# Performance work log

Hardware: AMD Instinct MI355X
Metric: run time of the kernel (lower is better)

Reference implementation:

```python
import jax, jax.numpy as jnp
import numpy as np

B, S, D, H = 2, 2048, 1024, 16
HD = D // H  # head_dim = 64


def setup_inputs() -> dict:
    rng = jax.random.key(0)
    ks = jax.random.split(rng, 14)
    s = 0.02
    return {
        "query": jax.random.normal(ks[0], (B, S, D), jnp.float32),
        "key": jax.random.normal(ks[1], (B, S, D), jnp.float32),
        "value": jax.random.normal(ks[2], (B, S, D), jnp.float32),
        "Wq": jax.random.normal(ks[3], (D, D), jnp.float32) * s,
        "bq": jnp.zeros((D,), jnp.float32),
        "Wk": jax.random.normal(ks[4], (D, D), jnp.float32) * s,
        "bk": jnp.zeros((D,), jnp.float32),
        "Wv": jax.random.normal(ks[5], (D, D), jnp.float32) * s,
        "bv": jnp.zeros((D,), jnp.float32),
        "Wo": jax.random.normal(ks[6], (D, D), jnp.float32) * s,
        "bo": jnp.zeros((D,), jnp.float32),
        "Wa": jax.random.normal(ks[7], (3, D, D), jnp.float32) * s,  # 3 aspect projections
        "ba": jnp.zeros((3, D), jnp.float32),
    }


def reference(query, key, value, Wq, bq, Wk, bk, Wv, bv, Wo, bo, Wa, ba):
    scale = 1.0 / jnp.sqrt(jnp.asarray(HD, query.dtype))
    # projections; split heads -> [B, H, S, HD]
    q = (query @ Wq + bq).reshape(B, S, H, HD).transpose(0, 2, 1, 3)
    k = (key @ Wk + bk).reshape(B, S, H, HD).transpose(0, 2, 1, 3)
    v = (value @ Wv + bv).reshape(B, S, H, HD).transpose(0, 2, 1, 3)
    # main attention (dropout p=0, no masks)
    logits = jnp.einsum('bhqd,bhkd->bhqk', q, k) * scale
    attn_weights = jax.nn.softmax(logits, axis=-1)  # [B, H, S, S]
    ctx = jnp.einsum('bhqk,bhkd->bhqd', attn_weights, v)
    attn_output = ctx.transpose(0, 2, 1, 3).reshape(B, S, D) @ Wo + bo
    # 3 interpretable aspect patterns: each proj applied to query and key,
    # full-dim QK^T scaled by sqrt(head_dim), softmax over keys.
    q_asp = jnp.einsum('bsd,ade->abse', query, Wa) + ba[:, None, None, :]
    k_asp = jnp.einsum('bsd,ade->abse', key, Wa) + ba[:, None, None, :]
    pat_logits = jnp.einsum('abqd,abkd->abqk', q_asp, k_asp) * scale
    patterns = jax.nn.softmax(pat_logits, axis=-1)  # [3, B, S, S]
    return attn_output, attn_weights, patterns
```

## Files before the change

### kernel.cpp

```cpp
#include <hip/hip_runtime.h>

typedef unsigned short u16;
typedef short s16x4 __attribute__((ext_vector_type(4)));
typedef short s16x8 __attribute__((ext_vector_type(8)));
typedef float f32x4 __attribute__((ext_vector_type(4)));

#define DEVFN __device__ __forceinline__

constexpr long AW_OFF  = 4194304;
constexpr long PAT_OFF = AW_OFF + 134217728;

DEVFN u16 f2bf(float x) {
  unsigned u = __builtin_bit_cast(unsigned, x);
  unsigned r = (u + 0x7fffu + ((u >> 16) & 1u)) >> 16;
  return (u16)r;
}

DEVFN void gld16(const u16* g, u16* l) {
  __builtin_amdgcn_global_load_lds(
      (const __attribute__((address_space(1))) unsigned int*)g,
      (__attribute__((address_space(3))) unsigned int*)l, 16, 0, 0);
}

__global__ __launch_bounds__(256) void k_cvt3(const float* __restrict__ a,
                                              const float* __restrict__ b,
                                              const float* __restrict__ c,
                                              u16* __restrict__ out, int n4) {
  int i = blockIdx.x * 256 + threadIdx.x;
  if (i >= n4) return;
  const float* in = (blockIdx.y == 0) ? a : (blockIdx.y == 1) ? b : c;
  float4 v = ((const float4*)in)[i];
  s16x4 o; o[0] = f2bf(v.x); o[1] = f2bf(v.y); o[2] = f2bf(v.z); o[3] = f2bf(v.w);
  ((s16x4*)(out + (long)blockIdx.y * 4194304))[i] = o;
}

__global__ __launch_bounds__(256) void k_pack3(const float* __restrict__ a,
                                               const float* __restrict__ b,
                                               const float* __restrict__ c,
                                               float* __restrict__ out) {
  int i = blockIdx.x * 256 + threadIdx.x;
  const float* in = (i < 1024) ? a : (i < 2048) ? b : c;
  out[i] = in[i & 1023];
}

__global__ __launch_bounds__(256) void k_trW(const float* __restrict__ Wq,
                                             const float* __restrict__ Wk,
                                             const float* __restrict__ Wv,
                                             const float* __restrict__ Wo,
                                             const float* __restrict__ Wa,
                                             u16* __restrict__ Wqt,
                                             u16* __restrict__ Wot,
                                             u16* __restrict__ Wat) {
  __shared__ u16 tile[32][33];
  const int z = blockIdx.z;
  const float* in;
  u16* outp;
  if (z == 0)      { in = Wq; outp = Wqt; }
  else if (z == 1) { in = Wk; outp = Wqt + 1048576; }
  else if (z == 2) { in = Wv; outp = Wqt + 2097152; }
  else if (z == 3) { in = Wo; outp = Wot; }
  else             { in = Wa + (long)(z - 4) * 1048576; outp = Wat + (long)(z - 4) * 1048576; }
  int k0 = blockIdx.y * 32, n0 = blockIdx.x * 32;
  int tx = threadIdx.x & 31, ty = threadIdx.x >> 5;
#pragma unroll
  for (int i = 0; i < 4; ++i)
    tile[ty + i * 8][tx] = f2bf(in[(long)(k0 + ty + i * 8) * 1024 + (n0 + tx)]);
  __syncthreads();
#pragma unroll
  for (int i = 0; i < 4; ++i)
    outp[(long)(n0 + ty + i * 8) * 1024 + (k0 + tx)] = tile[tx][ty + i * 8];
}

template <bool IN_F32>
__global__ __launch_bounds__(256) void k_tr(const void* __restrict__ inv,
                                            u16* __restrict__ out,
                                            long ldin, long ldout,
                                            long inz1, long inz2, long outz, int zdiv) {
  __shared__ u16 tile[32][33];
  int z = blockIdx.z;
  long ioff = (long)(z / zdiv) * inz1 + (long)(z % zdiv) * inz2;
  int k0 = blockIdx.y * 32, n0 = blockIdx.x * 32;
  int tx = threadIdx.x, ty = threadIdx.y;
#pragma unroll
  for (int i = 0; i < 4; ++i) {
    long k = k0 + ty + i * 8, n = n0 + tx;
    u16 v;
    if constexpr (IN_F32) v = f2bf(((const float*)inv)[ioff + k * ldin + n]);
    else                  v = ((const u16*)inv)[ioff + k * ldin + n];
    tile[ty + i * 8][tx] = v;
  }
  __syncthreads();
  long ooff = (long)z * outz;
#pragma unroll
  for (int i = 0; i < 4; ++i) {
    long n = n0 + ty + i * 8, k = k0 + tx;
    out[ooff + n * ldout + k] = tile[tx][ty + i * 8];
  }
}

template <typename OutT, int EPI>
__global__ __launch_bounds__(256) void k_gemm_nt(
    const u16* __restrict__ Ap, const u16* __restrict__ Bp, OutT* __restrict__ Cp,
    const float* __restrict__ bias, const float* __restrict__ rinv, float alpha, int K,
    long lda, long ldb, long ldc,
    long saz1, long saz2, long sbz1, long sbz2, long scz1, long scz2,
    long sbias, int zdiv) {
  __shared__ __align__(16) u16 At[128][64];
  __shared__ __align__(16) u16 Bt[128][64];
  const int tid = threadIdx.x, lane = tid & 63, wid = tid >> 6;
  const int wm = wid >> 1, wn = wid & 1;

  const int gx = gridDim.x, gy = gridDim.y;
  int id = (blockIdx.z * gy + blockIdx.y) * gx + blockIdx.x;
  const int nb = gx * gy * (int)gridDim.z;
  if ((nb & 7) == 0) id = (id & 7) * (nb >> 3) + (id >> 3);
  const int bxi = id % gx, byi = (id / gx) % gy, bzi = id / (gx * gy);

  const int z = bzi, z1 = z / zdiv, z2 = z % zdiv;
  const u16* Ab = Ap + (long)z1 * saz1 + (long)z2 * saz2;
  const u16* Bb = Bp + (long)z1 * sbz1 + (long)z2 * sbz2;
  OutT* C = Cp + (long)z1 * scz1 + (long)z2 * scz2;
  const float* bv = bias ? bias + (long)z2 * sbias : nullptr;
  const int row0 = byi * 128, col0 = bxi * 128;
  const int lk = lane & 15, g = lane >> 4;

  f32x4 acc[4][4] = {};

  for (int k0 = 0; k0 < K; k0 += 64) {
#pragma unroll
    for (int it = 0; it < 4; ++it) {
      const int u = it * 256 + tid;
      const int r = u >> 3, p = u & 7;
      const int cg = (p ^ (r & 7)) * 8;
      gld16(Ab + (long)(row0 + r) * lda + (k0 + cg), &At[r][p * 8]);
      gld16(Bb + (long)(col0 + r) * ldb + (k0 + cg), &Bt[r][p * 8]);
    }
    __syncthreads();
#pragma unroll
    for (int kk = 0; kk < 2; ++kk) {
      s16x8 af[4], bf[4];
#pragma unroll
      for (int m = 0; m < 4; ++m)
        af[m] = *(const s16x8*)&At[wm * 64 + m * 16 + lk][((kk * 4 + g) ^ (lk & 7)) * 8];
#pragma unroll
      for (int n = 0; n < 4; ++n)
        bf[n] = *(const s16x8*)&Bt[wn * 64 + n * 16 + lk][((kk * 4 + g) ^ (lk & 7)) * 8];
#pragma unroll
      for (int m = 0; m < 4; ++m)
#pragma unroll
        for (int n = 0; n < 4; ++n)
          acc[m][n] = __builtin_amdgcn_mfma_f32_16x16x32_bf16(af[m], bf[n], acc[m][n], 0, 0, 0);
    }
    __syncthreads();
  }

  const float* rz = (EPI == 1) ? rinv + (long)z * 2048 : nullptr;
#pragma unroll
  for (int m = 0; m < 4; ++m) {
    const int grow = row0 + wm * 64 + m * 16 + g * 4;
#pragma unroll
    for (int r = 0; r < 4; ++r) {
      float iv = 0.0f;
      if constexpr (EPI == 1) iv = rz[grow + r];
#pragma unroll
      for (int n = 0; n < 4; ++n) {
        const int gcol = col0 + wn * 64 + n * 16 + lk;
        float v;
        if constexpr (EPI == 1) v = __expf(alpha * acc[m][n][r]) * iv;
        else                    v = alpha * acc[m][n][r] + (bv ? bv[gcol] : 0.0f);
        if constexpr (sizeof(OutT) == 2) C[(long)(grow + r) * ldc + gcol] = f2bf(v);
        else                             C[(long)(grow + r) * ldc + gcol] = v;
      }
    }
  }
}

template <typename OutT, int EPI>
__global__ __launch_bounds__(512, 1) void k_gemm8(
    const u16* __restrict__ Ap, const u16* __restrict__ Bp, OutT* __restrict__ Cp,
    const float* __restrict__ bias, const float* __restrict__ rinv, float alpha, int K,
    long lda, long ldb, long ldc,
    long saz1, long saz2, long sbz1, long sbz2, long scz1, long scz2,
    long sbias, int zdiv) {
  extern __shared__ __align__(16) u16 dyn[];
  u16* At = dyn;
  u16* Bt = dyn + 32768;
  const int tid = threadIdx.x, lane = tid & 63, wid = tid >> 6;
  const int wm = wid >> 2, wn = wid & 3;

  const int gx = gridDim.x, gy = gridDim.y;
  int id = (blockIdx.z * gy + blockIdx.y) * gx + blockIdx.x;
  const int nb = gx * gy * (int)gridDim.z;
  if ((nb & 7) == 0) id = (id & 7) * (nb >> 3) + (id >> 3);
  const int bxi = id % gx, byi = (id / gx) % gy, bzi = id / (gx * gy);

  const int z = bzi, z1 = z / zdiv, z2 = z % zdiv;
  const u16* Ab = Ap + (long)z1 * saz1 + (long)z2 * saz2;
  const u16* Bb = Bp + (long)z1 * sbz1 + (long)z2 * sbz2;
  OutT* C = Cp + (long)z1 * scz1 + (long)z2 * scz2;
  const float* bv = bias ? bias + (long)z2 * sbias : nullptr;
  const int row0 = byi * 256, col0 = bxi * 256;
  const int lk = lane & 15, g = lane >> 4;

  f32x4 acc[8][4] = {};
  const int NT = K >> 6;

  auto STAGE = [&](int t, int b) {
    const int k0 = t << 6;
#pragma unroll
    for (int it = 0; it < 4; ++it) {
      const int u = it * 512 + tid;
      const int r = u >> 3, p = u & 7;
      const int cg = (p ^ (r & 7)) * 8;
      gld16(Ab + (long)(row0 + r) * lda + (k0 + cg), At + b * 16384 + r * 64 + p * 8);
      gld16(Bb + (long)(col0 + r) * ldb + (k0 + cg), Bt + b * 16384 + r * 64 + p * 8);
    }
  };

  STAGE(0, 0);
  STAGE(1, 1);
  for (int t = 0; t < NT; ++t) {
    if (t + 1 < NT) asm volatile("s_waitcnt vmcnt(8)" ::: "memory");
    else            asm volatile("s_waitcnt vmcnt(0)" ::: "memory");
    __builtin_amdgcn_sched_barrier(0);
    __builtin_amdgcn_s_barrier();
    __builtin_amdgcn_sched_barrier(0);
    const u16* Ax = At + (t & 1) * 16384;
    const u16* Bx = Bt + (t & 1) * 16384;
#pragma unroll
    for (int kk = 0; kk < 2; ++kk) {
      s16x8 af[8], bf[4];
#pragma unroll
      for (int m = 0; m < 8; ++m)
        af[m] = *(const s16x8*)(Ax + (wm * 128 + m * 16 + lk) * 64 + ((kk * 4 + g) ^ (lk & 7)) * 8);
#pragma unroll
      for (int n = 0; n < 4; ++n)
        bf[n] = *(const s16x8*)(Bx + (wn * 64 + n * 16 + lk) * 64 + ((kk * 4 + g) ^ (lk & 7)) * 8);
#pragma unroll
      for (int m = 0; m < 8; ++m)
#pragma unroll
        for (int n = 0; n < 4; ++n)
          acc[m][n] = __builtin_amdgcn_mfma_f32_16x16x32_bf16(af[m], bf[n], acc[m][n], 0, 0, 0);
    }
    __builtin_amdgcn_sched_barrier(0);
    __builtin_amdgcn_s_barrier();
    __builtin_amdgcn_sched_barrier(0);
    if (t + 2 < NT) STAGE(t + 2, t & 1);
  }

  const float* rz = (EPI == 1) ? rinv + (long)z * 2048 : nullptr;
#pragma unroll
  for (int m = 0; m < 8; ++m) {
    const int grow = row0 + wm * 128 + m * 16 + g * 4;
#pragma unroll
    for (int r = 0; r < 4; ++r) {
      float iv = 0.0f;
      if constexpr (EPI == 1) iv = rz[grow + r];
#pragma unroll
      for (int n = 0; n < 4; ++n) {
        const int gcol = col0 + wn * 64 + n * 16 + lk;
        float v;
        if constexpr (EPI == 1) v = __expf(alpha * acc[m][n][r]) * iv;
        else                    v = alpha * acc[m][n][r] + (bv ? bv[gcol] : 0.0f);
        if constexpr (sizeof(OutT) == 2) C[(long)(grow + r) * ldc + gcol] = f2bf(v);
        else                             C[(long)(grow + r) * ldc + gcol] = v;
      }
    }
  }
}

__global__ __launch_bounds__(256) void k_flash(
    const u16* __restrict__ qp, const u16* __restrict__ kp, const u16* __restrict__ vt,
    u16* __restrict__ ctx, float* __restrict__ rinv) {
  __shared__ __align__(16) char lds[49152];
  u16* Qt = (u16*)lds;
  u16* Kt = (u16*)(lds + 16384);
  u16* Vl = (u16*)(lds + 32768);
  const int tid = threadIdx.x, lane = tid & 63, wid = tid >> 6;
  const int wk = wid >> 1, wq = wid & 1;

  const int gx = gridDim.x;
  int id = blockIdx.y * gx + blockIdx.x;
  const int nb = gx * (int)gridDim.y;
  if ((nb & 7) == 0) id = (id & 7) * (nb >> 3) + (id >> 3);
  const int bh = id / gx, q0 = (id % gx) * 128;

  const long qkbase = (long)(bh >> 4) * 2097152 + (long)(bh & 15) * 64;
  const long vbase = (long)bh * 131072;
  const int lk = lane & 15, g = lane >> 4;
  const int sp = lane & 7;
  const int sr = lane >> 3;

#pragma unroll
  for (int i = 0; i < 4; ++i) {
    const int rr = (wid * 4 + i) * 8 + sr;
    gld16(qp + qkbase + (long)(q0 + rr) * 1024 + ((sp ^ (rr & 7)) * 8), Qt + rr * 64 + sp * 8);
  }
  __syncthreads();

  s16x8 qf[2][4];
#pragma unroll
  for (int kk = 0; kk < 2; ++kk) {
#pragma unroll
    for (int nq = 0; nq < 4; ++nq)
      qf[kk][nq] = *(const s16x8*)(Qt + (wq * 64 + nq * 16 + lk) * 64 + ((kk * 4 + g) ^ (lk & 7)) * 8);
  }

  f32x4 cacc[4][4] = {};
  float rs[4] = {0.f, 0.f, 0.f, 0.f};

  for (int t = 0; t < 16; ++t) {
    const int kb = t * 128;
#pragma unroll
    for (int i = 0; i < 4; ++i) {
      const int rr = (wid * 4 + i) * 8 + sr;
      gld16(kp + qkbase + (long)(kb + rr) * 1024 + ((sp ^ (rr & 7)) * 8), Kt + rr * 64 + sp * 8);
      const int dd = (wid * 4 + i) * 4 + g;
      const int pv = lane & 15;
      const int cv = (pv & 8) | ((pv ^ dd) & 7);
      gld16(vt + vbase + (long)dd * 2048 + (kb + cv * 8), Vl + dd * 128 + pv * 8);
    }
    __syncthreads();

    f32x4 st[4][4] = {};
#pragma unroll
    for (int kk = 0; kk < 2; ++kk) {
      s16x8 af[4];
#pragma unroll
      for (int mk = 0; mk < 4; ++mk)
        af[mk] = *(const s16x8*)(Kt + (wk * 64 + mk * 16 + lk) * 64 + ((kk * 4 + g) ^ (lk & 7)) * 8);
#pragma unroll
      for (int mk = 0; mk < 4; ++mk)
#pragma unroll
        for (int nq = 0; nq < 4; ++nq)
          st[mk][nq] = __builtin_amdgcn_mfma_f32_16x16x32_bf16(af[mk], qf[kk][nq], st[mk][nq], 0, 0, 0);
    }
#pragma unroll
    for (int mk = 0; mk < 4; ++mk)
#pragma unroll
      for (int nq = 0; nq < 4; ++nq)
#pragma unroll
        for (int j = 0; j < 4; ++j) {
          const float p = __expf(st[mk][nq][j] * 0.125f);
          st[mk][nq][j] = p;
          rs[nq] += p;
        }
#pragma unroll
    for (int ks = 0; ks < 2; ++ks) {
      s16x8 pb[4];
#pragma unroll
      for (int nq = 0; nq < 4; ++nq) {
        s16x8 b;
#pragma unroll
        for (int j = 0; j < 4; ++j) {
          b[j]     = (short)f2bf(st[2 * ks][nq][j]);
          b[4 + j] = (short)f2bf(st[2 * ks + 1][nq][j]);
        }
        pb[nq] = b;
      }
#pragma unroll
      for (int md = 0; md < 4; ++md) {
        const int rowv = md * 16 + lk;
        const int u0 = ks * 4 + (g >> 1);
        const int p0 = wk * 8 + ((u0 ^ (rowv & 7)) & 7);
        const int p2 = wk * 8 + (((u0 + 2) ^ (rowv & 7)) & 7);
        const u16* vb0 = Vl + rowv * 128 + p0 * 8 + (g & 1) * 4;
        const u16* vb2 = Vl + rowv * 128 + p2 * 8 + (g & 1) * 4;
        s16x4 lo = *(const s16x4*)vb0;
        s16x4 hi = *(const s16x4*)vb2;
        s16x8 vf;
        vf[0] = lo[0]; vf[1] = lo[1]; vf[2] = lo[2]; vf[3] = lo[3];
        vf[4] = hi[0]; vf[5] = hi[1]; vf[6] = hi[2]; vf[7] = hi[3];
#pragma unroll
        for (int nq = 0; nq < 4; ++nq)
          cacc[md][nq] = __builtin_amdgcn_mfma_f32_16x16x32_bf16(vf, pb[nq], cacc[md][nq], 0, 0, 0);
      }
    }
    __syncthreads();
  }

#pragma unroll
  for (int nq = 0; nq < 4; ++nq) {
    rs[nq] += __shfl_xor(rs[nq], 16, 64);
    rs[nq] += __shfl_xor(rs[nq], 32, 64);
  }
  float* ctxl = (float*)lds;
  float* rsl  = (float*)(lds + 33024);
  if (wk == 1) {
#pragma unroll
    for (int md = 0; md < 4; ++md)
#pragma unroll
      for (int nq = 0; nq < 4; ++nq)
#pragma unroll
        for (int r = 0; r < 4; ++r)
          ctxl[(md * 16 + g * 4 + r) * 129 + wq * 64 + nq * 16 + lk] = cacc[md][nq][r];
    if (lane < 16)
#pragma unroll
      for (int nq = 0; nq < 4; ++nq) rsl[wq * 64 + nq * 16 + lane] = rs[nq];
  }
  __syncthreads();
  if (wk == 0) {
#pragma unroll
    for (int md = 0; md < 4; ++md)
#pragma unroll
      for (int nq = 0; nq < 4; ++nq)
#pragma unroll
        for (int r = 0; r < 4; ++r) {
          const int idx = (md * 16 + g * 4 + r) * 129 + wq * 64 + nq * 16 + lk;
          ctxl[idx] += cacc[md][nq][r];
        }
    if (lane < 16)
#pragma unroll
      for (int nq = 0; nq < 4; ++nq) {
        const int qi = wq * 64 + nq * 16 + lane;
        const float inv = 1.0f / (rsl[qi] + rs[nq]);
        rsl[qi] = inv;
        rinv[(long)bh * 2048 + q0 + qi] = inv;
      }
  }
  __syncthreads();
  const int qr = tid >> 1, half = tid & 1;
  const float inv = rsl[qr];
  u16* dst = ctx + (long)(bh >> 4) * 2097152 + (long)(q0 + qr) * 1024 + (long)(bh & 15) * 64 + half * 32;
#pragma unroll
  for (int c = 0; c < 4; ++c) {
    s16x8 o;
#pragma unroll
    for (int j = 0; j < 8; ++j) {
      const int d = half * 32 + c * 8 + j;
      o[j] = (short)f2bf(ctxl[d * 129 + qr] * inv);
    }
    ((s16x8*)dst)[c] = o;
  }
}

__global__ __launch_bounds__(256) void k_softmax(float* __restrict__ base) {
  float* p = base + (long)blockIdx.x * 2048;
  const int t = threadIdx.x;
  float4 v0 = ((const float4*)p)[t];
  float4 v1 = ((const float4*)p)[t + 256];
  float m = fmaxf(fmaxf(fmaxf(v0.x, v0.y), fmaxf(v0.z, v0.w)),
                  fmaxf(fmaxf(v1.x, v1.y), fmaxf(v1.z, v1.w)));
#pragma unroll
  for (int i = 32; i >= 1; i >>= 1) m = fmaxf(m, __shfl_xor(m, i, 64));
  __shared__ float sm[4], ss[4];
  if ((t & 63) == 0) sm[t >> 6] = m;
  __syncthreads();
  m = fmaxf(fmaxf(sm[0], sm[1]), fmaxf(sm[2], sm[3]));
  float4 e0, e1;
  e0.x = __expf(v0.x - m); e0.y = __expf(v0.y - m); e0.z = __expf(v0.z - m); e0.w = __expf(v0.w - m);
  e1.x = __expf(v1.x - m); e1.y = __expf(v1.y - m); e1.z = __expf(v1.z - m); e1.w = __expf(v1.w - m);
  float s = (e0.x + e0.y + e0.z + e0.w) + (e1.x + e1.y + e1.z + e1.w);
#pragma unroll
  for (int i = 32; i >= 1; i >>= 1) s += __shfl_xor(s, i, 64);
  if ((t & 63) == 0) ss[t >> 6] = s;
  __syncthreads();
  s = ss[0] + ss[1] + ss[2] + ss[3];
  float inv = 1.0f / s;
  e0.x *= inv; e0.y *= inv; e0.z *= inv; e0.w *= inv;
  e1.x *= inv; e1.y *= inv; e1.z *= inv; e1.w *= inv;
  ((float4*)p)[t] = e0;
  ((float4*)p)[t + 256] = e1;
}

extern "C" void kernel_launch(void* const* d_in, const int* in_sizes, int n_in,
                              void* d_out, int out_size, void* d_ws, size_t ws_size,
                              hipStream_t stream) {
  const float* query = (const float*)d_in[0];
  const float* key   = (const float*)d_in[1];
  const float* value = (const float*)d_in[2];
  const float* Wq = (const float*)d_in[3];
  const float* bq = (const float*)d_in[4];
  const float* Wk = (const float*)d_in[5];
  const float* bk = (const float*)d_in[6];
  const float* Wv = (const float*)d_in[7];
  const float* bv = (const float*)d_in[8];
  const float* Wo = (const float*)d_in[9];
  const float* bo = (const float*)d_in[10];
  const float* Wa = (const float*)d_in[11];
  const float* ba = (const float*)d_in[12];
  float* out = (float*)d_out;
  char* ws = (char*)d_ws;

  u16* qb  = (u16*)(ws + 0);
  u16* Wqt = (u16*)(ws + 25165824);
  u16* Wot = (u16*)(ws + 31457280);
  u16* Wat = (u16*)(ws + 33554432);
  u16* qp  = (u16*)(ws + 39845888);
  u16* kp  = (u16*)(ws + 48234496);
  u16* vp  = (u16*)(ws + 56623104);
  u16* vt  = (u16*)(ws + 65011712);
  u16* ctx = (u16*)(ws + 73400320);
  u16* qa  = (u16*)(ws + 81788928);
  float* rinv  = (float*)(ws + 25165824);
  float* pbias = (float*)(ws + 132120576);

  hipFuncSetAttribute((const void*)k_gemm8<u16, 0>,
                      hipFuncAttributeMaxDynamicSharedMemorySize, 131072);
  hipFuncSetAttribute((const void*)k_gemm8<float, 0>,
                      hipFuncAttributeMaxDynamicSharedMemorySize, 131072);

  dim3 b256(256), b512(512);
  dim3 trb(32, 8);

  k_cvt3<<<dim3(4096, 3), b256, 0, stream>>>(query, key, value, qb, 1048576);
  k_pack3<<<12, b256, 0, stream>>>(bq, bk, bv, pbias);

  k_trW<<<dim3(32, 32, 7), b256, 0, stream>>>(Wq, Wk, Wv, Wo, Wa, Wqt, Wot, Wat);

  k_gemm8<u16, 0><<<dim3(4, 16, 3), b512, 131072, stream>>>(
      qb, Wqt, qp, pbias, nullptr, 1.0f, 1024, 1024, 1024, 1024,
      0, 4194304, 0, 1048576, 0, 4194304, 1024, 3);

  k_gemm8<u16, 0><<<dim3(4, 16, 6), b512, 131072, stream>>>(
      qb, Wat, qa, ba, nullptr, 1.0f, 1024, 1024, 1024, 1024,
      4194304, 0, 0, 1048576, 12582912, 4194304, 1024, 3);

  k_tr<false><<<dim3(2, 64, 32), trb, 0, stream>>>(
      vp, vt, 1024, 2048, 2097152, 64, 131072, 16);

  k_flash<<<dim3(16, 32), b256, 0, stream>>>(qp, kp, vt, ctx, rinv);

  k_gemm_nt<float, 1><<<dim3(16, 16, 32), b256, 0, stream>>>(
      qp, kp, out + AW_OFF, nullptr, rinv, 0.125f, 64, 1024, 1024, 2048,
      2097152, 64, 2097152, 64, 67108864, 4194304, 0, 16);

  k_gemm8<float, 0><<<dim3(8, 8, 6), b512, 131072, stream>>>(
      qa, qa + 12582912, out + PAT_OFF, nullptr, nullptr, 0.125f, 1024, 1024, 1024, 2048,
      0, 2097152, 0, 2097152, 0, 4194304, 0, 6);

  k_softmax<<<12288, b256, 0, stream>>>(out + PAT_OFF);

  k_gemm8<float, 0><<<dim3(4, 16, 1), b512, 131072, stream>>>(
      ctx, Wot, out, bo, nullptr, 1.0f, 1024, 1024, 1024, 1024,
      0, 0, 0, 0, 0, 0, 0, 1);
}
```

Before: 539.9 us.

## Replace 256x256 GEMM with triple-buffered 256x128 kernel, use exp2 in softmax

Replaces the double-buffered 256x256-tile GEMM with a triple-buffered 256x128-tile variant that uses 8 waves in a 4x2 layout, issues two stages ahead and raises wave priority around the MFMA block. The QKV and output projections move to the smaller existing k_gemm_nt kernel so their grids fill more CUs. Exponentials in the flash and attention-weight epilogues become exp2f with a prefolded log2e*scale constant. The aim is more blocks in flight and better latency hiding for the large pattern GEMM. The cost is lower per-block reuse and more LDS per block.

Measured after the change: 508.2 us. 5.9% less time.

```diff
diff --git a/kernel.cpp b/kernel.cpp
--- a/kernel.cpp
+++ b/kernel.cpp
@@ -9,6 +9,7 @@
 
 constexpr long AW_OFF  = 4194304;
 constexpr long PAT_OFF = AW_OFF + 134217728;
+constexpr float EXPSC  = 0.18033688011f;
 
 DEVFN u16 f2bf(float x) {
   unsigned u = __builtin_bit_cast(unsigned, x);
@@ -166,7 +167,7 @@
       for (int n = 0; n < 4; ++n) {
         const int gcol = col0 + wn * 64 + n * 16 + lk;
         float v;
-        if constexpr (EPI == 1) v = __expf(alpha * acc[m][n][r]) * iv;
+        if constexpr (EPI == 1) v = exp2f(acc[m][n][r] * EXPSC) * iv;
         else                    v = alpha * acc[m][n][r] + (bv ? bv[gcol] : 0.0f);
         if constexpr (sizeof(OutT) == 2) C[(long)(grow + r) * ldc + gcol] = f2bf(v);
         else                             C[(long)(grow + r) * ldc + gcol] = v;
@@ -175,18 +176,16 @@
   }
 }
 
-template <typename OutT, int EPI>
-__global__ __launch_bounds__(512, 1) void k_gemm8(
+template <typename OutT, bool BIAS>
+__global__ __launch_bounds__(512, 1) void k_gemm3p(
     const u16* __restrict__ Ap, const u16* __restrict__ Bp, OutT* __restrict__ Cp,
-    const float* __restrict__ bias, const float* __restrict__ rinv, float alpha, int K,
+    const float* __restrict__ bias, float alpha, int K,
     long lda, long ldb, long ldc,
     long saz1, long saz2, long sbz1, long sbz2, long scz1, long scz2,
     long sbias, int zdiv) {
   extern __shared__ __align__(16) u16 dyn[];
-  u16* At = dyn;
-  u16* Bt = dyn + 32768;
   const int tid = threadIdx.x, lane = tid & 63, wid = tid >> 6;
-  const int wm = wid >> 2, wn = wid & 3;
+  const int wm = wid >> 1, wn = wid & 1;
 
   const int gx = gridDim.x, gy = gridDim.y;
   int id = (blockIdx.z * gy + blockIdx.y) * gx + blockIdx.x;
@@ -198,70 +197,77 @@
   const u16* Ab = Ap + (long)z1 * saz1 + (long)z2 * saz2;
   const u16* Bb = Bp + (long)z1 * sbz1 + (long)z2 * sbz2;
   OutT* C = Cp + (long)z1 * scz1 + (long)z2 * scz2;
-  const float* bv = bias ? bias + (long)z2 * sbias : nullptr;
-  const int row0 = byi * 256, col0 = bxi * 256;
+  const float* bv = BIAS ? bias + (long)z2 * sbias : nullptr;
+  const int row0 = byi * 256, col0 = bxi * 128;
   const int lk = lane & 15, g = lane >> 4;
 
-  f32x4 acc[8][4] = {};
+  f32x4 acc[4][4] = {};
   const int NT = K >> 6;
 
-  auto STAGE = [&](int t, int b) {
+  auto STAGE = [&](int t, int bi) {
     const int k0 = t << 6;
+    u16* Ax = dyn + bi * 24576;
+    u16* Bx = dyn + bi * 24576 + 16384;
 #pragma unroll
     for (int it = 0; it < 4; ++it) {
       const int u = it * 512 + tid;
       const int r = u >> 3, p = u & 7;
       const int cg = (p ^ (r & 7)) * 8;
-      gld16(Ab + (long)(row0 + r) * lda + (k0 + cg), At + b * 16384 + r * 64 + p * 8);
-      gld16(Bb + (long)(col0 + r) * ldb + (k0 + cg), Bt + b * 16384 + r * 64 + p * 8);
+      gld16(Ab + (long)(row0 + r) * lda + (k0 + cg), Ax + r * 64 + p * 8);
+    }
+#pragma unroll
+    for (int it = 0; it < 2; ++it) {
+      const int u = it * 512 + tid;
+      const int r = u >> 3, p = u & 7;
+      const int cg = (p ^ (r & 7)) * 8;
+      gld16(Bb + (long)(col0 + r) * ldb + (k0 + cg), Bx + r * 64 + p * 8);
     }
   };
 
-  STAGE(0, 0);
-  STAGE(1, 1);
+  STAGE(0, 0); STAGE(1, 1); STAGE(2, 2);
+  int bi = 0;
   for (int t = 0; t < NT; ++t) {
-    if (t + 1 < NT) asm volatile("s_waitcnt vmcnt(8)" ::: "memory");
-    else            asm volatile("s_waitcnt vmcnt(0)" ::: "memory");
+    if (t + 2 < NT)      asm volatile("s_waitcnt vmcnt(12)" ::: "memory");
+    else if (t + 1 < NT) asm volatile("s_waitcnt vmcnt(6)" ::: "memory");
+    else                 asm volatile("s_waitcnt vmcnt(0)" ::: "memory");
     __builtin_amdgcn_sched_barrier(0);
     __builtin_amdgcn_s_barrier();
     __builtin_amdgcn_sched_barrier(0);
-    const u16* Ax = At + (t & 1) * 16384;
-    const u16* Bx = Bt + (t & 1) * 16384;
+    const u16* Ax = dyn + bi * 24576;
+    const u16* Bx = dyn + bi * 24576 + 16384;
 #pragma unroll
     for (int kk = 0; kk < 2; ++kk) {
-      s16x8 af[8], bf[4];
-#pragma unroll
-      for (int m = 0; m < 8; ++m)
-        af[m] = *(const s16x8*)(Ax + (wm * 128 + m * 16 + lk) * 64 + ((kk * 4 + g) ^ (lk & 7)) * 8);
+      s16x8 af[4], bf[4];
+#pragma unroll
+      for (int m = 0; m < 4; ++m)
+        af[m] = *(const s16x8*)(Ax + (wm * 64 + m * 16 + lk) * 64 + ((kk * 4 + g) ^ (lk & 7)) * 8);
 #pragma unroll
       for (int n = 0; n < 4; ++n)
         bf[n] = *(const s16x8*)(Bx + (wn * 64 + n * 16 + lk) * 64 + ((kk * 4 + g) ^ (lk & 7)) * 8);
-#pragma unroll
-      for (int m = 0; m < 8; ++m)
+      __builtin_amdgcn_s_setprio(1);
+#pragma unroll
+      for (int m = 0; m < 4; ++m)
 #pragma unroll
         for (int n = 0; n < 4; ++n)
           acc[m][n] = __builtin_amdgcn_mfma_f32_16x16x32_bf16(af[m], bf[n], acc[m][n], 0, 0, 0);
+      __builtin_amdgcn_s_setprio(0);
     }
     __builtin_amdgcn_sched_barrier(0);
     __builtin_amdgcn_s_barrier();
     __builtin_amdgcn_sched_barrier(0);
-    if (t + 2 < NT) STAGE(t + 2, t & 1);
-  }
-
-  const float* rz = (EPI == 1) ? rinv + (long)z * 2048 : nullptr;
-#pragma unroll
-  for (int m = 0; m < 8; ++m) {
-    const int grow = row0 + wm * 128 + m * 16 + g * 4;
+    if (t + 3 < NT) STAGE(t + 3, bi);
+    bi = (bi == 2) ? 0 : bi + 1;
+  }
+
+#pragma unroll
+  for (int m = 0; m < 4; ++m) {
+    const int grow = row0 + wm * 64 + m * 16 + g * 4;
 #pragma unroll
     for (int r = 0; r < 4; ++r) {
-      float iv = 0.0f;
-      if constexpr (EPI == 1) iv = rz[grow + r];
 #pragma unroll
       for (int n = 0; n < 4; ++n) {
         const int gcol = col0 + wn * 64 + n * 16 + lk;
-        float v;
-        if constexpr (EPI == 1) v = __expf(alpha * acc[m][n][r]) * iv;
-        else                    v = alpha * acc[m][n][r] + (bv ? bv[gcol] : 0.0f);
+        float v = alpha * acc[m][n][r] + (BIAS ? bv[gcol] : 0.0f);
         if constexpr (sizeof(OutT) == 2) C[(long)(grow + r) * ldc + gcol] = f2bf(v);
         else                             C[(long)(grow + r) * ldc + gcol] = v;
       }
@@ -341,7 +347,7 @@
       for (int nq = 0; nq < 4; ++nq)
 #pragma unroll
         for (int j = 0; j < 4; ++j) {
-          const float p = __expf(st[mk][nq][j] * 0.125f);
+          const float p = exp2f(st[mk][nq][j] * EXPSC);
           st[mk][nq][j] = p;
           rs[nq] += p;
         }
@@ -495,10 +501,10 @@
   float* rinv  = (float*)(ws + 25165824);
   float* pbias = (float*)(ws + 132120576);
 
-  hipFuncSetAttribute((const void*)k_gemm8<u16, 0>,
-                      hipFuncAttributeMaxDynamicSharedMemorySize, 131072);
-  hipFuncSetAttribute((const void*)k_gemm8<float, 0>,
-                      hipFuncAttributeMaxDynamicSharedMemorySize, 131072);
+  hipFuncSetAttribute((const void*)k_gemm3p<u16, true>,
+                      hipFuncAttributeMaxDynamicSharedMemorySize, 147456);
+  hipFuncSetAttribute((const void*)k_gemm3p<float, false>,
+                      hipFuncAttributeMaxDynamicSharedMemorySize, 147456);
 
   dim3 b256(256), b512(512);
   dim3 trb(32, 8);
@@ -508,12 +514,12 @@
 
   k_trW<<<dim3(32, 32, 7), b256, 0, stream>>>(Wq, Wk, Wv, Wo, Wa, Wqt, Wot, Wat);
 
-  k_gemm8<u16, 0><<<dim3(4, 16, 3), b512, 131072, stream>>>(
+  k_gemm_nt<u16, 0><<<dim3(8, 32, 3), b256, 0, stream>>>(
       qb, Wqt, qp, pbias, nullptr, 1.0f, 1024, 1024, 1024, 1024,
       0, 4194304, 0, 1048576, 0, 4194304, 1024, 3);
 
-  k_gemm8<u16, 0><<<dim3(4, 16, 6), b512, 131072, stream>>>(
-      qb, Wat, qa, ba, nullptr, 1.0f, 1024, 1024, 1024, 1024,
+  k_gemm3p<u16, true><<<dim3(8, 16, 6), b512, 147456, stream>>>(
+      qb, Wat, qa, ba, 1.0f, 1024, 1024, 1024, 1024,
       4194304, 0, 0, 1048576, 12582912, 4194304, 1024, 3);
 
   k_tr<false><<<dim3(2, 64, 32), trb, 0, stream>>>(
@@ -525,13 +531,12 @@
       qp, kp, out + AW_OFF, nullptr, rinv, 0.125f, 64, 1024, 1024, 2048,
       2097152, 64, 2097152, 64, 67108864, 4194304, 0, 16);
 
-  k_gemm8<float, 0><<<dim3(8, 8, 6), b512, 131072, stream>>>(
-      qa, qa + 12582912, out + PAT_OFF, nullptr, nullptr, 0.125f, 1024, 1024, 1024, 2048,
+  k_gemm3p<float, false><<<dim3(16, 8, 6), b512, 147456, stream>>>(
+      qa, qa + 12582912, out + PAT_OFF, nullptr, 0.125f, 1024, 1024, 1024, 2048,
       0, 2097152, 0, 2097152, 0, 4194304, 0, 6);
 
   k_softmax<<<12288, b256, 0, stream>>>(out + PAT_OFF);
 
-  k_gemm8<float, 0><<<dim3(4, 16, 1), b512, 131072, stream>>>(
-      ctx, Wot, out, bo, nullptr, 1.0f, 1024, 1024, 1024, 1024,
-      0, 0, 0, 0, 0, 0, 0, 1);
-}
+  k_gemm_nt<float, 0><<<dim3(8, 32, 1), b256, 0, stream>>>(
+      ctx, Wot, out, bo, nullptr, 1.0f, 1024, 1024, 1024, 1024, 0, 0, 0, 0, 0, 0, 0, 1);
+}
```
